# Performance work log

Hardware: AMD Instinct MI355X
Metric: run time of the kernel (lower is better)

Reference implementation:

```python
import jax, jax.numpy as jnp
import numpy as np

NUM_ROI = 148
P = 1
Q = 5
N = 131072


def setup_inputs() -> dict:
    key = jax.random.key(0)
    kX, kZ, kWr, kbr, kWf, kbf = jax.random.split(key, 6)
    X = jax.random.normal(kX, (N, P), dtype=jnp.float32)
    Z = jax.random.normal(kZ, (N, Q), dtype=jnp.float32)
    # Stacked per-ROI linear layers (torch nn.Linear default init scale)
    s_r = 1.0 / np.sqrt(Q)
    s_f = 1.0 / np.sqrt(P + Q)
    Wr = jax.random.uniform(kWr, (NUM_ROI, Q), jnp.float32, -s_r, s_r)
    br = jax.random.uniform(kbr, (NUM_ROI,), jnp.float32, -s_r, s_r)
    Wf = jax.random.uniform(kWf, (NUM_ROI, P + Q), jnp.float32, -s_f, s_f)
    bf = jax.random.uniform(kbf, (NUM_ROI,), jnp.float32, -s_f, s_f)
    return {"X": X, "Z": Z, "Wr": Wr, "br": br, "Wf": Wf, "bf": bf}


def reference(X, Z, Wr, br, Wf, bf):
    # combined_XZ: [N, p+q]
    XZ = jnp.concatenate([X, Z], axis=-1)
    # All 148 per-ROI GEMVs batched into two matmuls; output stacked as [roi, N]
    r_out = jnp.einsum("nq,rq->rn", Z, Wr) + br[:, None]   # [148, N]
    f_out = jnp.einsum("nd,rd->rn", XZ, Wf) + bf[:, None]  # [148, N]
    return (r_out, f_out)
```

## Files before the change

### kernel.cpp

```cpp
#include <hip/hip_runtime.h>

#define NUM_ROI 148
#define NQ 5
#define NN 131072
#define ROI_SPLIT 4
#define ROI_PER (NUM_ROI / ROI_SPLIT)

__global__ __launch_bounds__(256) void coconet_kernel(
    const float* __restrict__ X, const float* __restrict__ Z,
    const float* __restrict__ Wr, const float* __restrict__ br,
    const float* __restrict__ Wf, const float* __restrict__ bf,
    float* __restrict__ out)
{
    __shared__ float w[ROI_PER][16];
    const int tid = threadIdx.x;
    const int roiBase = blockIdx.y * ROI_PER;

    if (tid < ROI_PER) {
        const int r = roiBase + tid;
        #pragma unroll
        for (int q = 0; q < NQ; ++q) w[tid][q] = Wr[r * NQ + q];
        w[tid][5] = br[r];
        #pragma unroll
        for (int d = 0; d < 6; ++d) w[tid][6 + d] = Wf[r * 6 + d];
        w[tid][12] = bf[r];
    }
    __syncthreads();

    const int n0 = (blockIdx.x * 256 + tid) * 4;

    const float4 x4 = *reinterpret_cast<const float4*>(X + n0);
    const float x[4] = {x4.x, x4.y, x4.z, x4.w};

    float z[4][NQ];
    {
        const float4* zp = reinterpret_cast<const float4*>(Z + (size_t)n0 * NQ);
        const float4 a = zp[0], b = zp[1], c = zp[2], d = zp[3], e = zp[4];
        const float tmp[20] = {a.x, a.y, a.z, a.w, b.x, b.y, b.z, b.w,
                               c.x, c.y, c.z, c.w, d.x, d.y, d.z, d.w,
                               e.x, e.y, e.z, e.w};
        #pragma unroll
        for (int j = 0; j < 4; ++j)
            #pragma unroll
            for (int q = 0; q < NQ; ++q) z[j][q] = tmp[j * NQ + q];
    }

    float* outR = out + (size_t)roiBase * NN + n0;
    float* outF = out + (size_t)(NUM_ROI + roiBase) * NN + n0;

    for (int i = 0; i < ROI_PER; ++i) {
        const float4 w0 = *reinterpret_cast<const float4*>(&w[i][0]);
        const float4 w1 = *reinterpret_cast<const float4*>(&w[i][4]);
        const float4 w2 = *reinterpret_cast<const float4*>(&w[i][8]);
        const float bfv = w[i][12];
        const float wr[NQ] = {w0.x, w0.y, w0.z, w0.w, w1.x};
        const float brv = w1.y, wfx = w1.z;
        const float wf[NQ] = {w1.w, w2.x, w2.y, w2.z, w2.w};

        float rr[4], ff[4];
        #pragma unroll
        for (int j = 0; j < 4; ++j) {
            float r_ = brv;
            float f_ = fmaf(x[j], wfx, bfv);
            #pragma unroll
            for (int q = 0; q < NQ; ++q) {
                r_ = fmaf(z[j][q], wr[q], r_);
                f_ = fmaf(z[j][q], wf[q], f_);
            }
            rr[j] = r_;
            ff[j] = f_;
        }
        *reinterpret_cast<float4*>(outR) = make_float4(rr[0], rr[1], rr[2], rr[3]);
        *reinterpret_cast<float4*>(outF) = make_float4(ff[0], ff[1], ff[2], ff[3]);
        outR += NN;
        outF += NN;
    }
}

extern "C" void kernel_launch(void* const* d_in, const int* in_sizes, int n_in,
                              void* d_out, int out_size, void* d_ws, size_t ws_size,
                              hipStream_t stream) {
    const float* X  = (const float*)d_in[0];
    const float* Z  = (const float*)d_in[1];
    const float* Wr = (const float*)d_in[2];
    const float* br = (const float*)d_in[3];
    const float* Wf = (const float*)d_in[4];
    const float* bf = (const float*)d_in[5];
    float* out = (float*)d_out;

    dim3 grid(NN / (256 * 4), ROI_SPLIT);
    coconet_kernel<<<grid, 256, 0, stream>>>(X, Z, Wr, br, Wf, bf, out);
}
```

Baseline: 162.6 us.

## Assign one ROI per block and loop over N segments

Changes the grid from splitting ROIs into four groups with shared-memory weights to one block per ROI and 8 N-segments, with weights held in registers. Each thread iterates over 16 strided chunks of N, reloading Z and X for every ROI. This is meant to raise block count and give more independent loads and stores in flight, with no shared memory or syncs. The trade-off is that input reads now rely on cache reuse across ROIs.

```diff
diff --git a/kernel.cpp b/kernel.cpp
--- a/kernel.cpp
+++ b/kernel.cpp
@@ -3,8 +3,9 @@
 #define NUM_ROI 148
 #define NQ 5
 #define NN 131072
-#define ROI_SPLIT 4
-#define ROI_PER (NUM_ROI / ROI_SPLIT)
+#define NSEG 8
+#define SEGF (NN / NSEG)
+#define ITERS (SEGF / (256 * 4))
 
 __global__ __launch_bounds__(256) void coconet_kernel(
     const float* __restrict__ X, const float* __restrict__ Z,
@@ -12,68 +13,55 @@
     const float* __restrict__ Wf, const float* __restrict__ bf,
     float* __restrict__ out)
 {
-    __shared__ float w[ROI_PER][16];
+    const int roi = blockIdx.y;
     const int tid = threadIdx.x;
-    const int roiBase = blockIdx.y * ROI_PER;
+    const int nbase = blockIdx.x * SEGF + tid * 4;
 
-    if (tid < ROI_PER) {
-        const int r = roiBase + tid;
-        #pragma unroll
-        for (int q = 0; q < NQ; ++q) w[tid][q] = Wr[r * NQ + q];
-        w[tid][5] = br[r];
-        #pragma unroll
-        for (int d = 0; d < 6; ++d) w[tid][6 + d] = Wf[r * 6 + d];
-        w[tid][12] = bf[r];
-    }
-    __syncthreads();
+    const float wr0 = Wr[roi * NQ + 0], wr1 = Wr[roi * NQ + 1],
+                wr2 = Wr[roi * NQ + 2], wr3 = Wr[roi * NQ + 3],
+                wr4 = Wr[roi * NQ + 4];
+    const float brv = br[roi];
+    const float wfx = Wf[roi * 6 + 0];
+    const float wf0 = Wf[roi * 6 + 1], wf1 = Wf[roi * 6 + 2],
+                wf2 = Wf[roi * 6 + 3], wf3 = Wf[roi * 6 + 4],
+                wf4 = Wf[roi * 6 + 5];
+    const float bfv = bf[roi];
 
-    const int n0 = (blockIdx.x * 256 + tid) * 4;
+    float* oR = out + (size_t)roi * NN + nbase;
+    float* oF = out + (size_t)(NUM_ROI + roi) * NN + nbase;
 
-    const float4 x4 = *reinterpret_cast<const float4*>(X + n0);
-    const float x[4] = {x4.x, x4.y, x4.z, x4.w};
+    #pragma unroll 4
+    for (int it = 0; it < ITERS; ++it) {
+        const int n = nbase + it * 1024;
 
-    float z[4][NQ];
-    {
-        const float4* zp = reinterpret_cast<const float4*>(Z + (size_t)n0 * NQ);
-        const float4 a = zp[0], b = zp[1], c = zp[2], d = zp[3], e = zp[4];
-        const float tmp[20] = {a.x, a.y, a.z, a.w, b.x, b.y, b.z, b.w,
-                               c.x, c.y, c.z, c.w, d.x, d.y, d.z, d.w,
-                               e.x, e.y, e.z, e.w};
-        #pragma unroll
-        for (int j = 0; j < 4; ++j)
-            #pragma unroll
-            for (int q = 0; q < NQ; ++q) z[j][q] = tmp[j * NQ + q];
-    }
-
-    float* outR = out + (size_t)roiBase * NN + n0;
-    float* outF = out + (size_t)(NUM_ROI + roiBase) * NN + n0;
-
-    for (int i = 0; i < ROI_PER; ++i) {
-        const float4 w0 = *reinterpret_cast<const float4*>(&w[i][0]);
-        const float4 w1 = *reinterpret_cast<const float4*>(&w[i][4]);
-        const float4 w2 = *reinterpret_cast<const float4*>(&w[i][8]);
-        const float bfv = w[i][12];
-        const float wr[NQ] = {w0.x, w0.y, w0.z, w0.w, w1.x};
-        const float brv = w1.y, wfx = w1.z;
-        const float wf[NQ] = {w1.w, w2.x, w2.y, w2.z, w2.w};
+        const float4* zp = reinterpret_cast<const float4*>(Z + (size_t)n * NQ);
+        const float4 a = zp[0], b2 = zp[1], c = zp[2], d = zp[3], e = zp[4];
+        const float4 x4 = *reinterpret_cast<const float4*>(X + n);
+        const float x[4] = {x4.x, x4.y, x4.z, x4.w};
+        const float t[20] = {a.x,  a.y,  a.z,  a.w,  b2.x, b2.y, b2.z, b2.w,
+                             c.x,  c.y,  c.z,  c.w,  d.x,  d.y,  d.z,  d.w,
+                             e.x,  e.y,  e.z,  e.w};
 
         float rr[4], ff[4];
         #pragma unroll
         for (int j = 0; j < 4; ++j) {
+            const float z0 = t[j * 5 + 0], z1 = t[j * 5 + 1],
+                        z2 = t[j * 5 + 2], z3 = t[j * 5 + 3],
+                        z4 = t[j * 5 + 4];
             float r_ = brv;
             float f_ = fmaf(x[j], wfx, bfv);
-            #pragma unroll
-            for (int q = 0; q < NQ; ++q) {
-                r_ = fmaf(z[j][q], wr[q], r_);
-                f_ = fmaf(z[j][q], wf[q], f_);
-            }
+            r_ = fmaf(z0, wr0, r_);  f_ = fmaf(z0, wf0, f_);
+            r_ = fmaf(z1, wr1, r_);  f_ = fmaf(z1, wf1, f_);
+            r_ = fmaf(z2, wr2, r_);  f_ = fmaf(z2, wf2, f_);
+            r_ = fmaf(z3, wr3, r_);  f_ = fmaf(z3, wf3, f_);
+            r_ = fmaf(z4, wr4, r_);  f_ = fmaf(z4, wf4, f_);
             rr[j] = r_;
             ff[j] = f_;
         }
-        *reinterpret_cast<float4*>(outR) = make_float4(rr[0], rr[1], rr[2], rr[3]);
-        *reinterpret_cast<float4*>(outF) = make_float4(ff[0], ff[1], ff[2], ff[3]);
-        outR += NN;
-        outF += NN;
+        *reinterpret_cast<float4*>(oR + it * 1024) =
+            make_float4(rr[0], rr[1], rr[2], rr[3]);
+        *reinterpret_cast<float4*>(oF + it * 1024) =
+            make_float4(ff[0], ff[1], ff[2], ff[3]);
     }
 }
 
@@ -88,6 +76,6 @@
     const float* bf = (const float*)d_in[5];
     float* out = (float*)d_out;
 
-    dim3 grid(NN / (256 * 4), ROI_SPLIT);
+    dim3 grid(NSEG, NUM_ROI);
     coconet_kernel<<<grid, 256, 0, stream>>>(X, Z, Wr, br, Wf, bf, out);
 }
```

New measurement: 190.7 us. 17.2% more time.
